# Kernel tuning notes

Hardware: AMD Instinct MI355X
Metric: run time of the kernel (lower is better)

The kernel has to match this reference:

```python
import jax, jax.numpy as jnp
import numpy as np

T, I, H = 30, 100, 256  # seq_len, input_size, hidden_size (hard-coded in the module)


def setup_inputs() -> dict:
    key = jax.random.key(0)
    ks = jax.random.split(key, 16)
    B = 512
    N = B * 10  # LSTM batch after view(-1, 30, 100)
    w = lambda k, shape: (jax.random.normal(k, shape, dtype=jnp.float32) * 0.05)
    return {
        "x": jax.random.normal(ks[0], (B, 10, T, I), dtype=jnp.float32),
        "h0": jax.random.normal(ks[1], (2, N, H), dtype=jnp.float32),
        "c0": jax.random.normal(ks[2], (2, N, H), dtype=jnp.float32),
        # PyTorch LSTM params, gate order i,f,g,o; forward and backward directions
        "W_ih_f": w(ks[3], (4 * H, I)),
        "W_hh_f": w(ks[4], (4 * H, H)),
        "b_ih_f": w(ks[5], (4 * H,)),
        "b_hh_f": w(ks[6], (4 * H,)),
        "W_ih_b": w(ks[7], (4 * H, I)),
        "W_hh_b": w(ks[8], (4 * H, H)),
        "b_ih_b": w(ks[9], (4 * H,)),
        "b_hh_b": w(ks[10], (4 * H,)),
        # head: Linear(2560,64) -> Dropout(eval: identity) -> Linear(64,5) -> Softmax
        "W1": w(ks[11], (64, 10 * 256)),
        "b1": w(ks[12], (64,)),
        "W2": w(ks[13], (5, 64)),
        "b2": w(ks[14], (5,)),
    }


def _run_dir(xg, h, c, W_hh):
    """Scan an LSTM direction. xg: [T, N, 4H] precomputed input gates. Returns final h."""
    def step(carry, g_x):
        h, c = carry
        g = g_x + h @ W_hh.T
        i, f, gg, o = jnp.split(g, 4, axis=-1)
        c = jax.nn.sigmoid(f) * c + jax.nn.sigmoid(i) * jnp.tanh(gg)
        h = jax.nn.sigmoid(o) * jnp.tanh(c)
        return (h, c), None
    (h, c), _ = jax.lax.scan(step, (h, c), xg)
    return h


def reference(x, h0, c0, W_ih_f, W_hh_f, b_ih_f, b_hh_f,
              W_ih_b, W_hh_b, b_ih_b, b_hh_b, W1, b1, W2, b2):
    B = x.shape[0]
    xr = x.reshape(-1, T, I)              # [N, 30, 100]
    xs = jnp.transpose(xr, (1, 0, 2))     # [T, N, I] time-major
    # precompute input contributions to gates for all timesteps (one big GEMM)
    xg_f = jnp.einsum('tni,gi->tng', xs, W_ih_f) + b_ih_f + b_hh_f
    xg_b = jnp.einsum('tni,gi->tng', xs[::-1], W_ih_b) + b_ih_b + b_hh_b
    hF = _run_dir(xg_f, h0[0], c0[0], W_hh_f)  # fwd hidden at t=T-1 -> output[:, -1, :256]
    hB = _run_dir(xg_b, h0[1], c0[1], W_hh_b)  # bwd hidden at t=0  -> output[:, 0, 256:]
    # output[:, -1, :128] = hF[:, :128]; output[:, 0, -128:] = hB[:, 128:256]
    x_fea = jnp.concatenate(
        [hF[:, :128].reshape(B, 10, 128), hB[:, 128:256].reshape(B, 10, 128)], axis=-1)
    flat = x_fea.reshape(B, -1)           # [B, 2560]
    z = flat @ W1.T + b1                  # Dropout(0.5) is identity in eval
    logits = z @ W2.T + b2
    y_pred = jax.nn.softmax(logits, axis=-1)
    return (y_pred, x_fea)
```

## Files before the change

### kernel.cpp

```cpp
#include <hip/hip_runtime.h>

typedef __bf16 bf16_t;
typedef __bf16 bf16x8 __attribute__((ext_vector_type(8)));
typedef float f32x4 __attribute__((ext_vector_type(4)));
typedef unsigned long long u64;

#define TSEQ 30
#define ISZ  100
#define HSZ  256
#define NB   5120
#define BATCH 512
#define G4   1024
#define TILE 320
#define NBGRP 16
#define CH   10240
#define SLABX (4 * CH)
#define SLABH (8 * CH)

__device__ __forceinline__ float fsig(float x)  { return 1.0f / (1.0f + __expf(-x)); }
__device__ __forceinline__ float ftanh(float x) { return 2.0f / (1.0f + __expf(-2.0f * x)) - 1.0f; }

__global__ void prep_weights(const float* __restrict__ Wih_f, const float* __restrict__ Whh_f,
                             const float* __restrict__ bih_f, const float* __restrict__ bhh_f,
                             const float* __restrict__ Wih_b, const float* __restrict__ Whh_b,
                             const float* __restrict__ bih_b, const float* __restrict__ bhh_b,
                             bf16_t* __restrict__ Wf, float* __restrict__ bias)
{
    int idx = blockIdx.x * 256 + threadIdx.x;
    if (idx >= 2 * G4 * 384) return;
    int d = idx / (G4 * 384);
    int r = (idx / 384) % G4;
    int k = idx % 384;
    int h = r >> 2, gate = r & 3;
    int grow = gate * HSZ + h;
    const float* Wih = d ? Wih_b : Wih_f;
    const float* Whh = d ? Whh_b : Whh_f;
    float v;
    if (k < ISZ)       v = Wih[grow * ISZ + k];
    else if (k < 128)  v = 0.0f;
    else               v = Whh[grow * HSZ + (k - 128)];
    int mf = r >> 4, lr = r & 15;
    int ks = k >> 5, lq = (k >> 3) & 3, e = k & 7;
    size_t o = ((((size_t)d * 64 + mf) * 12 + ks) * 64 + lq * 16 + lr) * 8 + e;
    Wf[o] = (bf16_t)v;
    if (k == 0) {
        const float* bih = d ? bih_b : bih_f;
        const float* bhh = d ? bhh_b : bhh_f;
        bias[d * G4 + r] = bih[grow] + bhh[grow];
    }
}

__global__ void prep_x(const float* __restrict__ x, bf16_t* __restrict__ xBf)
{
    int idx = blockIdx.x * 256 + threadIdx.x;
    if (idx >= NBGRP * TSEQ * SLABX) return;
    int e    = idx & 7;
    int lane = (idx >> 3) & 63;
    int i2   = idx >> 9;
    int nblk = i2 % 20; i2 /= 20;
    int ks   = i2 & 3;  i2 >>= 2;
    int t    = i2 % TSEQ;
    int bgrp = i2 / TSEQ;
    int n = bgrp * TILE + nblk * 16 + (lane & 15);
    int k = ks * 32 + (lane >> 4) * 8 + e;
    float v = (k < ISZ) ? x[(size_t)n * (TSEQ * ISZ) + t * ISZ + k] : 0.0f;
    xBf[idx] = (bf16_t)v;
}

__global__ void prep_state(const float* __restrict__ h0, bf16_t* __restrict__ hA)
{
    int idx = blockIdx.x * 256 + threadIdx.x;
    if (idx >= 2 * NBGRP * SLABH) return;
    int e    = idx & 7;
    int lane = (idx >> 3) & 63;
    int i2   = idx >> 9;
    int nblk = i2 % 20; i2 /= 20;
    int ksh  = i2 & 7;  i2 >>= 3;
    int bgrp = i2 & 15;
    int dir  = i2 >> 4;
    int col = bgrp * TILE + nblk * 16 + (lane & 15);
    int hid = ksh * 32 + (lane >> 4) * 8 + e;
    hA[idx] = (bf16_t)h0[((size_t)dir * NB + col) * HSZ + hid];
}

__global__ void prep_c(const float* __restrict__ c0, float* __restrict__ cws)
{
    int idx = blockIdx.x * 256 + threadIdx.x;
    if (idx >= 256 * 512 * 20) return;
    int m   = idx & 3;
    int nf  = (idx >> 2) % 5;
    int tid = (idx / 20) & 511;
    int bid = idx / (20 * 512);
    int msub = bid >> 5, dir = (bid >> 4) & 1, bgrp = bid & 15;
    int lane = tid & 63, mw = (tid >> 6) >> 2, nw = (tid >> 6) & 3;
    int lr = lane & 15, lq = lane >> 4;
    int col = bgrp * TILE + nw * 80 + nf * 16 + lr;
    int hid = msub * 32 + mw * 16 + m * 4 + lq;
    cws[idx] = c0[((size_t)dir * NB + col) * HSZ + hid];
}

__global__ void prep_w1t(const float* __restrict__ W1, float* __restrict__ W1T)
{
    int idx = blockIdx.x * 256 + threadIdx.x;
    if (idx >= 2560 * 64) return;
    int k = idx / 64, j = idx % 64;
    W1T[k * 64 + j] = W1[j * 2560 + k];
}

__device__ __forceinline__ void wave_wait(unsigned* flag, unsigned tgt)
{
    if ((threadIdx.x & 63) == 0) {
        while (__hip_atomic_fetch_add(flag, 0u, __ATOMIC_RELAXED, __HIP_MEMORY_SCOPE_AGENT) < tgt)
            __builtin_amdgcn_s_sleep(1);
    }
    __builtin_amdgcn_wave_barrier();
    __builtin_amdgcn_sched_barrier(0);
}

template<bool FAST>
__device__ void run_steps(const bf16_t* __restrict__ xBf,
                          bf16_t* __restrict__ hA, bf16_t* __restrict__ hB,
                          bf16_t* __restrict__ hfin,
                          const bf16_t* wL, bf16_t* pkL, unsigned* flags,
                          f32x4* c4, const float4* bq,
                          int dir, int bgrp, int msub,
                          int tid, int lane, int mw, int nw, int lr, int lq)
{
    const unsigned fo = (unsigned)(nw * 5 * 512 + lane * 8);
    const bf16_t* wp = wL + (mw * 4 * 12) * 512 + lane * 8;

#pragma unroll 1
    for (int t = 0; t < TSEQ; ++t) {
        const bf16_t* hs = (t & 1) ? hB : hA;
        bf16_t*       hw = (t & 1) ? hA : hB;
        const int tx = dir ? (TSEQ - 1 - t) : t;
        const bf16_t* xp = xBf + (size_t)(bgrp * TSEQ + tx) * SLABX + fo;
        const bf16_t* hp = hs + (size_t)(dir * NBGRP + bgrp) * SLABH + fo;

        f32x4 acc[4][5] = {};
#pragma unroll
        for (int c = 0; c < 4; ++c) {
            bf16x8 b[5];
#pragma unroll
            for (int nf = 0; nf < 5; ++nf)
                b[nf] = *(const bf16x8*)(xp + nf * 512);
            bf16x8 a[4];
#pragma unroll
            for (int m = 0; m < 4; ++m)
                a[m] = *(const bf16x8*)(wp + (m * 12 + c) * 512);
#pragma unroll
            for (int m = 0; m < 4; ++m)
#pragma unroll
                for (int nf = 0; nf < 5; ++nf)
                    acc[m][nf] = __builtin_amdgcn_mfma_f32_16x16x32_bf16(a[m], b[nf], acc[m][nf], 0, 0, 0);
            xp += CH;
        }
        if (FAST)
            asm volatile("buffer_inv sc0" ::: "memory");
#pragma unroll
        for (int c = 0; c < 8; ++c) {
            if (c != msub) wave_wait(flags + c * 16, (unsigned)t);
            bf16x8 b[5];
#pragma unroll
            for (int nf = 0; nf < 5; ++nf) {
                const bf16_t* src = hp + nf * 512;
                if (FAST) {
                    b[nf] = *(const bf16x8*)src;
                } else {
                    union { u64 q[2]; bf16x8 v; } u;
                    u.q[0] = __hip_atomic_load((const u64*)src,       __ATOMIC_RELAXED, __HIP_MEMORY_SCOPE_AGENT);
                    u.q[1] = __hip_atomic_load((const u64*)(src + 4), __ATOMIC_RELAXED, __HIP_MEMORY_SCOPE_AGENT);
                    b[nf] = u.v;
                }
            }
            bf16x8 a[4];
#pragma unroll
            for (int m = 0; m < 4; ++m)
                a[m] = *(const bf16x8*)(wp + (m * 12 + c + 4) * 512);
#pragma unroll
            for (int m = 0; m < 4; ++m)
#pragma unroll
                for (int nf = 0; nf < 5; ++nf)
                    acc[m][nf] = __builtin_amdgcn_mfma_f32_16x16x32_bf16(a[m], b[nf], acc[m][nf], 0, 0, 0);
            hp += CH;
        }

        if (t < TSEQ - 1) {
#pragma unroll
            for (int m = 0; m < 4; ++m) {
                float4 bb = bq[m];
                int hl = mw * 16 + m * 4 + lq;
#pragma unroll
                for (int nf = 0; nf < 5; ++nf) {
                    f32x4 g = acc[m][nf];
                    float gi = fsig(g[0] + bb.x);
                    float gf = fsig(g[1] + bb.y);
                    float gz = ftanh(g[2] + bb.z);
                    float go = fsig(g[3] + bb.w);
                    float cn = gf * c4[nf][m] + gi * gz;
                    c4[nf][m] = cn;
                    pkL[(nw * 5 + nf) * 512 + ((hl >> 3) * 16 + lr) * 8 + (hl & 7)]
                        = (bf16_t)(go * ftanh(cn));
                }
            }
            __syncthreads();
            bf16_t* dstb = hw + (size_t)(dir * NBGRP + bgrp) * SLABH + (size_t)msub * CH;
            if (FAST) {
                uint4* dst = (uint4*)dstb;
                const uint4* src = (const uint4*)pkL;
                for (int i = tid; i < 1280; i += 512) dst[i] = src[i];
            } else {
                u64* dst = (u64*)dstb;
                const u64* src = (const u64*)pkL;
                for (int i = tid; i < 2560; i += 512)
                    __hip_atomic_store(&dst[i], src[i], __ATOMIC_RELAXED, __HIP_MEMORY_SCOPE_AGENT);
            }
            __syncthreads();
            if (tid == 0)
                __hip_atomic_fetch_add(flags + msub * 16, 1u,
                    FAST ? __ATOMIC_RELAXED : __ATOMIC_RELEASE, __HIP_MEMORY_SCOPE_AGENT);
        } else {
#pragma unroll
            for (int m = 0; m < 4; ++m) {
                float4 bb = bq[m];
#pragma unroll
                for (int nf = 0; nf < 5; ++nf) {
                    f32x4 g = acc[m][nf];
                    float gi = fsig(g[0] + bb.x);
                    float gf = fsig(g[1] + bb.y);
                    float gz = ftanh(g[2] + bb.z);
                    float go = fsig(g[3] + bb.w);
                    float cn = gf * c4[nf][m] + gi * gz;
                    float hn = go * ftanh(cn);
                    int col = bgrp * TILE + nw * 80 + nf * 16 + lr;
                    int hid = msub * 32 + mw * 16 + m * 4 + lq;
                    hfin[((size_t)dir * NB + col) * HSZ + hid] = (bf16_t)hn;
                }
            }
        }
    }
}

__global__ __launch_bounds__(512, 1)
void lstm_persist(const bf16_t* __restrict__ Wf, const float* __restrict__ bias,
                  const bf16_t* __restrict__ xBf, const float* __restrict__ cws,
                  bf16_t* __restrict__ hA, bf16_t* __restrict__ hB,
                  bf16_t* __restrict__ hfin, unsigned* __restrict__ bar,
                  unsigned* __restrict__ xccA)
{
    __shared__ __align__(16) bf16_t wL[8 * 12 * 512];
    __shared__ __align__(16) bf16_t pkL[CH];
    __shared__ int sFast;

    const int bid  = blockIdx.x;
    const int msub = bid >> 5;
    const int dir  = (bid >> 4) & 1;
    const int bgrp = bid & 15;
    const int tid  = threadIdx.x;
    const int lane = tid & 63;
    const int mw   = (tid >> 6) >> 2;
    const int nw   = (tid >> 6) & 3;
    const int lr   = lane & 15;
    const int lq   = lane >> 4;

    {
        const uint4* wsrc = (const uint4*)(Wf + ((size_t)dir * 64 + msub * 8) * 12 * 512);
        uint4* wdst = (uint4*)wL;
        for (int i = tid; i < 6144; i += 512) wdst[i] = wsrc[i];
    }
    const float* cp = cws + ((size_t)bid * 512 + tid) * 20;
    f32x4 c4[5];
#pragma unroll
    for (int nf = 0; nf < 5; ++nf) c4[nf] = *(const f32x4*)(cp + nf * 4);
    float4 bq[4];
#pragma unroll
    for (int m = 0; m < 4; ++m)
        bq[m] = *(const float4*)(bias + dir * G4 + (msub * 32 + mw * 16 + m * 4 + lq) * 4);

    unsigned* flags  = bar + (dir * NBGRP + bgrp) * 128;
    unsigned* mybarX = bar + 32 * 128 + (dir * NBGRP + bgrp) * 16;

    unsigned xcc;
    asm volatile("s_getreg_b32 %0, hwreg(HW_REG_XCC_ID)" : "=s"(xcc));
    if (tid == 0) {
        __hip_atomic_store(&xccA[bid], xcc, __ATOMIC_RELAXED, __HIP_MEMORY_SCOPE_AGENT);
        __hip_atomic_fetch_add(mybarX, 1u, __ATOMIC_RELEASE, __HIP_MEMORY_SCOPE_AGENT);
        while (__hip_atomic_fetch_add(mybarX, 0u, __ATOMIC_RELAXED, __HIP_MEMORY_SCOPE_AGENT) < 8u)
            __builtin_amdgcn_s_sleep(1);
        int ok = (xcc < 8u) ? 1 : 0;
        for (int m2 = 0; m2 < 8; ++m2) {
            unsigned v = __hip_atomic_load(&xccA[m2 * 32 + dir * 16 + bgrp],
                                           __ATOMIC_RELAXED, __HIP_MEMORY_SCOPE_AGENT);
            ok &= (v == xcc) ? 1 : 0;
        }
        sFast = ok;
    }
    __syncthreads();

    if (sFast)
        run_steps<true>(xBf, hA, hB, hfin, wL, pkL, flags, c4, bq,
                        dir, bgrp, msub, tid, lane, mw, nw, lr, lq);
    else
        run_steps<false>(xBf, hA, hB, hfin, wL, pkL, flags, c4, bq,
                         dir, bgrp, msub, tid, lane, mw, nw, lr, lq);
}

__global__ __launch_bounds__(256)
void head_kernel(const bf16_t* __restrict__ hfin, const float* __restrict__ W1T,
                 const float* __restrict__ b1, const float* __restrict__ W2,
                 const float* __restrict__ b2, float* __restrict__ out)
{
    __shared__ float flat_s[2560];
    __shared__ float partial[4][64];
    __shared__ float zs[64];
    __shared__ float ls[5];
    __shared__ float es[5];
    int b = blockIdx.x, tid = threadIdx.x;
    const bf16_t* hF = hfin;
    const bf16_t* hB = hfin + (size_t)NB * HSZ;
    float* xfea = out + BATCH * 5 + (size_t)b * 2560;

    for (int j = tid; j < 2560; j += 256) {
        int s = j >> 8, c = j & 255;
        int n = b * 10 + s;
        float v = (c < 128) ? (float)hF[(size_t)n * HSZ + c] : (float)hB[(size_t)n * HSZ + c];
        flat_s[j] = v;
        xfea[j] = v;
    }
    __syncthreads();
    int j = tid & 63, q = tid >> 6;
    float sum = 0.0f;
    for (int k = q * 640; k < (q + 1) * 640; ++k) sum += flat_s[k] * W1T[k * 64 + j];
    partial[q][j] = sum;
    __syncthreads();
    if (tid < 64) zs[tid] = partial[0][tid] + partial[1][tid] + partial[2][tid] + partial[3][tid] + b1[tid];
    __syncthreads();
    if (tid < 5) {
        float l = b2[tid];
        for (int k = 0; k < 64; ++k) l += zs[k] * W2[tid * 64 + k];
        ls[tid] = l;
    }
    __syncthreads();
    if (tid < 5) {
        float m = ls[0];
        for (int k = 1; k < 5; ++k) m = fmaxf(m, ls[k]);
        es[tid] = __expf(ls[tid] - m);
    }
    __syncthreads();
    if (tid < 5) {
        float s5 = es[0] + es[1] + es[2] + es[3] + es[4];
        out[b * 5 + tid] = es[tid] / s5;
    }
}

extern "C" void kernel_launch(void* const* d_in, const int* in_sizes, int n_in,
                              void* d_out, int out_size, void* d_ws, size_t ws_size,
                              hipStream_t stream) {
    const float* x     = (const float*)d_in[0];
    const float* h0    = (const float*)d_in[1];
    const float* c0    = (const float*)d_in[2];
    const float* Wih_f = (const float*)d_in[3];
    const float* Whh_f = (const float*)d_in[4];
    const float* bih_f = (const float*)d_in[5];
    const float* bhh_f = (const float*)d_in[6];
    const float* Wih_b = (const float*)d_in[7];
    const float* Whh_b = (const float*)d_in[8];
    const float* bih_b = (const float*)d_in[9];
    const float* bhh_b = (const float*)d_in[10];
    const float* W1    = (const float*)d_in[11];
    const float* b1    = (const float*)d_in[12];
    const float* W2    = (const float*)d_in[13];
    const float* b2    = (const float*)d_in[14];
    float* out = (float*)d_out;

    uintptr_t ws = (uintptr_t)d_ws;
    bf16_t*   Wf   = (bf16_t*)(ws);
    float*    bias = (float*)(ws + 1572864);
    bf16_t*   xBf  = (bf16_t*)(ws + 1581056);
    bf16_t*   hAb  = (bf16_t*)(ws + 40902656);
    bf16_t*   hBb  = (bf16_t*)(ws + 46145536);
    bf16_t*   hfin = (bf16_t*)(ws + 51388416);
    float*    W1T  = (float*)(ws + 56631296);
    float*    cws  = (float*)(ws + 57286656);
    unsigned* bar  = (unsigned*)(ws + 67772416);
    unsigned* xccA = (unsigned*)(ws + 67790848);

    hipMemsetAsync((void*)bar, 0, 18432, stream);

    prep_weights<<<(2 * G4 * 384 + 255) / 256, 256, 0, stream>>>(
        Wih_f, Whh_f, bih_f, bhh_f, Wih_b, Whh_b, bih_b, bhh_b, Wf, bias);
    prep_x<<<(NBGRP * TSEQ * SLABX + 255) / 256, 256, 0, stream>>>(x, xBf);
    prep_state<<<(2 * NBGRP * SLABH + 255) / 256, 256, 0, stream>>>(h0, hAb);
    prep_c<<<(256 * 512 * 20 + 255) / 256, 256, 0, stream>>>(c0, cws);
    prep_w1t<<<(2560 * 64 + 255) / 256, 256, 0, stream>>>(W1, W1T);

    lstm_persist<<<256, 512, 0, stream>>>(Wf, bias, xBf, cws, hAb, hBb, hfin, bar, xccA);
    head_kernel<<<BATCH, 256, 0, stream>>>(hfin, W1T, b1, W2, b2, out);
}
```

Before: 467.0 us.

## Split blocks across both directions and replace per-chunk waits with per-wave flags

Each persistent block now handles both LSTM directions: half its threads work on forward and half on backward, each owning 16 hidden units instead of 32. Per-chunk flag waits become a single ballot-based batch wait over 16 per-wave flags. The LDS staging buffer and its two __syncthreads are dropped, and h values are written straight to global with a per-wave flag increment. This is meant to shorten the per-step cross-block synchronization path, at the cost of scattered 2-byte global stores and more flags to poll per step.

```diff
diff --git a/kernel.cpp b/kernel.cpp
--- a/kernel.cpp
+++ b/kernel.cpp
@@ -87,16 +87,19 @@
 {
     int idx = blockIdx.x * 256 + threadIdx.x;
     if (idx >= 256 * 512 * 20) return;
-    int m   = idx & 3;
-    int nf  = (idx >> 2) % 5;
-    int tid = (idx / 20) & 511;
-    int bid = idx / (20 * 512);
-    int msub = bid >> 5, dir = (bid >> 4) & 1, bgrp = bid & 15;
-    int lane = tid & 63, mw = (tid >> 6) >> 2, nw = (tid >> 6) & 3;
+    int cell = idx % 20;
+    int m    = cell / 10, nf = cell % 10;
+    int tid  = (idx / 20) & 511;
+    int bid  = idx / (20 * 512);
+    int msub = bid >> 4, bgrp = bid & 15;
+    int dirc = tid >> 8;
+    int ctid = tid & 255;
+    int wavec = ctid >> 6, lane = ctid & 63;
+    int mw = wavec >> 1, nw = wavec & 1;
     int lr = lane & 15, lq = lane >> 4;
-    int col = bgrp * TILE + nw * 80 + nf * 16 + lr;
-    int hid = msub * 32 + mw * 16 + m * 4 + lq;
-    cws[idx] = c0[((size_t)dir * NB + col) * HSZ + hid];
+    int col = bgrp * TILE + (nw * 10 + nf) * 16 + lr;
+    int hid = msub * 16 + mw * 8 + m * 4 + lq;
+    cws[idx] = c0[((size_t)dirc * NB + col) * HSZ + hid];
 }
 
 __global__ void prep_w1t(const float* __restrict__ W1, float* __restrict__ W1T)
@@ -107,13 +110,16 @@
     W1T[k * 64 + j] = W1[j * 2560 + k];
 }
 
-__device__ __forceinline__ void wave_wait(unsigned* flag, unsigned tgt)
-{
-    if ((threadIdx.x & 63) == 0) {
-        while (__hip_atomic_fetch_add(flag, 0u, __ATOMIC_RELAXED, __HIP_MEMORY_SCOPE_AGENT) < tgt)
-            __builtin_amdgcn_s_sleep(1);
-    }
-    __builtin_amdgcn_wave_barrier();
+__device__ __forceinline__ void batch_wait(unsigned* flags, unsigned tgt, int lane)
+{
+    while (true) {
+        unsigned v = tgt;
+        if (lane < 16)
+            v = __hip_atomic_fetch_add(flags + lane * 16, 0u,
+                                       __ATOMIC_RELAXED, __HIP_MEMORY_SCOPE_AGENT);
+        if (__ballot(v >= tgt) == ~0ull) break;
+        __builtin_amdgcn_s_sleep(8);
+    }
     __builtin_amdgcn_sched_barrier(0);
 }
 
@@ -121,48 +127,56 @@
 __device__ void run_steps(const bf16_t* __restrict__ xBf,
                           bf16_t* __restrict__ hA, bf16_t* __restrict__ hB,
                           bf16_t* __restrict__ hfin,
-                          const bf16_t* wL, bf16_t* pkL, unsigned* flags,
-                          f32x4* c4, const float4* bq,
-                          int dir, int bgrp, int msub,
+                          const bf16_t* wL, unsigned* myflags, unsigned* ownflag,
+                          float* cst, const float4* bq,
+                          int dirc, int bgrp, int msub,
                           int tid, int lane, int mw, int nw, int lr, int lq)
 {
-    const unsigned fo = (unsigned)(nw * 5 * 512 + lane * 8);
-    const bf16_t* wp = wL + (mw * 4 * 12) * 512 + lane * 8;
+    const unsigned fo = (unsigned)(nw * 10 * 512 + lane * 8);
+    const bf16_t* wp = wL + ((size_t)(dirc * 4 + mw * 2) * 12) * 512 + lane * 8;
+    const size_t slab = (size_t)(dirc * NBGRP + bgrp) * SLABH;
+
+    unsigned sb[2];
+#pragma unroll
+    for (int m = 0; m < 2; ++m) {
+        int hid = msub * 16 + mw * 8 + m * 4 + lq;
+        sb[m] = (unsigned)((hid >> 5) * CH + (((hid & 31) >> 3) * 16 + lr) * 8 + (hid & 7));
+    }
 
 #pragma unroll 1
     for (int t = 0; t < TSEQ; ++t) {
         const bf16_t* hs = (t & 1) ? hB : hA;
         bf16_t*       hw = (t & 1) ? hA : hB;
-        const int tx = dir ? (TSEQ - 1 - t) : t;
+        const int tx = dirc ? (TSEQ - 1 - t) : t;
         const bf16_t* xp = xBf + (size_t)(bgrp * TSEQ + tx) * SLABX + fo;
-        const bf16_t* hp = hs + (size_t)(dir * NBGRP + bgrp) * SLABH + fo;
-
-        f32x4 acc[4][5] = {};
+        const bf16_t* hp = hs + slab + fo;
+
+        f32x4 acc0[10] = {}, acc1[10] = {};
 #pragma unroll
         for (int c = 0; c < 4; ++c) {
-            bf16x8 b[5];
-#pragma unroll
-            for (int nf = 0; nf < 5; ++nf)
+            bf16x8 b[10];
+#pragma unroll
+            for (int nf = 0; nf < 10; ++nf)
                 b[nf] = *(const bf16x8*)(xp + nf * 512);
-            bf16x8 a[4];
-#pragma unroll
-            for (int m = 0; m < 4; ++m)
-                a[m] = *(const bf16x8*)(wp + (m * 12 + c) * 512);
-#pragma unroll
-            for (int m = 0; m < 4; ++m)
-#pragma unroll
-                for (int nf = 0; nf < 5; ++nf)
-                    acc[m][nf] = __builtin_amdgcn_mfma_f32_16x16x32_bf16(a[m], b[nf], acc[m][nf], 0, 0, 0);
+            bf16x8 a0 = *(const bf16x8*)(wp + (0 * 12 + c) * 512);
+            bf16x8 a1 = *(const bf16x8*)(wp + (1 * 12 + c) * 512);
+#pragma unroll
+            for (int nf = 0; nf < 10; ++nf) {
+                acc0[nf] = __builtin_amdgcn_mfma_f32_16x16x32_bf16(a0, b[nf], acc0[nf], 0, 0, 0);
+                acc1[nf] = __builtin_amdgcn_mfma_f32_16x16x32_bf16(a1, b[nf], acc1[nf], 0, 0, 0);
+            }
             xp += CH;
         }
+
+        batch_wait(myflags, 4u * (unsigned)t, lane);
         if (FAST)
             asm volatile("buffer_inv sc0" ::: "memory");
+
 #pragma unroll
         for (int c = 0; c < 8; ++c) {
-            if (c != msub) wave_wait(flags + c * 16, (unsigned)t);
-            bf16x8 b[5];
-#pragma unroll
-            for (int nf = 0; nf < 5; ++nf) {
+            bf16x8 b[10];
+#pragma unroll
+            for (int nf = 0; nf < 10; ++nf) {
                 const bf16_t* src = hp + nf * 512;
                 if (FAST) {
                     b[nf] = *(const bf16x8*)src;
@@ -173,68 +187,61 @@
                     b[nf] = u.v;
                 }
             }
-            bf16x8 a[4];
-#pragma unroll
-            for (int m = 0; m < 4; ++m)
-                a[m] = *(const bf16x8*)(wp + (m * 12 + c + 4) * 512);
-#pragma unroll
-            for (int m = 0; m < 4; ++m)
-#pragma unroll
-                for (int nf = 0; nf < 5; ++nf)
-                    acc[m][nf] = __builtin_amdgcn_mfma_f32_16x16x32_bf16(a[m], b[nf], acc[m][nf], 0, 0, 0);
+            bf16x8 a0 = *(const bf16x8*)(wp + (0 * 12 + 4 + c) * 512);
+            bf16x8 a1 = *(const bf16x8*)(wp + (1 * 12 + 4 + c) * 512);
+#pragma unroll
+            for (int nf = 0; nf < 10; ++nf) {
+                acc0[nf] = __builtin_amdgcn_mfma_f32_16x16x32_bf16(a0, b[nf], acc0[nf], 0, 0, 0);
+                acc1[nf] = __builtin_amdgcn_mfma_f32_16x16x32_bf16(a1, b[nf], acc1[nf], 0, 0, 0);
+            }
             hp += CH;
         }
 
         if (t < TSEQ - 1) {
-#pragma unroll
-            for (int m = 0; m < 4; ++m) {
+            bf16_t* hwp = hw + slab;
+#pragma unroll
+            for (int m = 0; m < 2; ++m) {
                 float4 bb = bq[m];
-                int hl = mw * 16 + m * 4 + lq;
-#pragma unroll
-                for (int nf = 0; nf < 5; ++nf) {
-                    f32x4 g = acc[m][nf];
+#pragma unroll
+                for (int nf = 0; nf < 10; ++nf) {
+                    f32x4 g = m ? acc1[nf] : acc0[nf];
                     float gi = fsig(g[0] + bb.x);
                     float gf = fsig(g[1] + bb.y);
                     float gz = ftanh(g[2] + bb.z);
                     float go = fsig(g[3] + bb.w);
-                    float cn = gf * c4[nf][m] + gi * gz;
-                    c4[nf][m] = cn;
-                    pkL[(nw * 5 + nf) * 512 + ((hl >> 3) * 16 + lr) * 8 + (hl & 7)]
-                        = (bf16_t)(go * ftanh(cn));
+                    float cn = gf * cst[m * 10 + nf] + gi * gz;
+                    cst[m * 10 + nf] = cn;
+                    bf16_t hv = (bf16_t)(go * ftanh(cn));
+                    unsigned off = sb[m] + (unsigned)((nw * 10 + nf) * 512);
+                    if (FAST) {
+                        hwp[off] = hv;
+                    } else {
+                        union { bf16_t h; unsigned short u; } cv; cv.h = hv;
+                        __hip_atomic_store((unsigned short*)(hwp + off), cv.u,
+                                           __ATOMIC_RELAXED, __HIP_MEMORY_SCOPE_AGENT);
+                    }
                 }
             }
-            __syncthreads();
-            bf16_t* dstb = hw + (size_t)(dir * NBGRP + bgrp) * SLABH + (size_t)msub * CH;
-            if (FAST) {
-                uint4* dst = (uint4*)dstb;
-                const uint4* src = (const uint4*)pkL;
-                for (int i = tid; i < 1280; i += 512) dst[i] = src[i];
-            } else {
-                u64* dst = (u64*)dstb;
-                const u64* src = (const u64*)pkL;
-                for (int i = tid; i < 2560; i += 512)
-                    __hip_atomic_store(&dst[i], src[i], __ATOMIC_RELAXED, __HIP_MEMORY_SCOPE_AGENT);
-            }
-            __syncthreads();
-            if (tid == 0)
-                __hip_atomic_fetch_add(flags + msub * 16, 1u,
+            if (FAST) asm volatile("s_waitcnt vmcnt(0)" ::: "memory");
+            if ((tid & 63) == 0)
+                __hip_atomic_fetch_add(ownflag, 1u,
                     FAST ? __ATOMIC_RELAXED : __ATOMIC_RELEASE, __HIP_MEMORY_SCOPE_AGENT);
         } else {
 #pragma unroll
-            for (int m = 0; m < 4; ++m) {
+            for (int m = 0; m < 2; ++m) {
                 float4 bb = bq[m];
-#pragma unroll
-                for (int nf = 0; nf < 5; ++nf) {
-                    f32x4 g = acc[m][nf];
+                int hid = msub * 16 + mw * 8 + m * 4 + lq;
+#pragma unroll
+                for (int nf = 0; nf < 10; ++nf) {
+                    f32x4 g = m ? acc1[nf] : acc0[nf];
                     float gi = fsig(g[0] + bb.x);
                     float gf = fsig(g[1] + bb.y);
                     float gz = ftanh(g[2] + bb.z);
                     float go = fsig(g[3] + bb.w);
-                    float cn = gf * c4[nf][m] + gi * gz;
+                    float cn = gf * cst[m * 10 + nf] + gi * gz;
                     float hn = go * ftanh(cn);
-                    int col = bgrp * TILE + nw * 80 + nf * 16 + lr;
-                    int hid = msub * 32 + mw * 16 + m * 4 + lq;
-                    hfin[((size_t)dir * NB + col) * HSZ + hid] = (bf16_t)hn;
+                    int col = bgrp * TILE + (nw * 10 + nf) * 16 + lr;
+                    hfin[((size_t)dirc * NB + col) * HSZ + hid] = (bf16_t)hn;
                 }
             }
         }
@@ -248,48 +255,59 @@
                   bf16_t* __restrict__ hfin, unsigned* __restrict__ bar,
                   unsigned* __restrict__ xccA)
 {
-    __shared__ __align__(16) bf16_t wL[8 * 12 * 512];
-    __shared__ __align__(16) bf16_t pkL[CH];
+    __shared__ __align__(16) bf16_t wL[2 * 4 * 12 * 512];
     __shared__ int sFast;
 
     const int bid  = blockIdx.x;
-    const int msub = bid >> 5;
-    const int dir  = (bid >> 4) & 1;
+    const int msub = bid >> 4;
     const int bgrp = bid & 15;
     const int tid  = threadIdx.x;
-    const int lane = tid & 63;
-    const int mw   = (tid >> 6) >> 2;
-    const int nw   = (tid >> 6) & 3;
+    const int dirc = tid >> 8;
+    const int ctid = tid & 255;
+    const int wavec = ctid >> 6;
+    const int lane = ctid & 63;
+    const int mw   = wavec >> 1;
+    const int nw   = wavec & 1;
     const int lr   = lane & 15;
     const int lq   = lane >> 4;
 
     {
-        const uint4* wsrc = (const uint4*)(Wf + ((size_t)dir * 64 + msub * 8) * 12 * 512);
         uint4* wdst = (uint4*)wL;
-        for (int i = tid; i < 6144; i += 512) wdst[i] = wsrc[i];
+        for (int i = tid; i < 6144; i += 512) {
+            int d = i / 3072, off = i % 3072;
+            const uint4* src = (const uint4*)(Wf + ((size_t)(d * 64 + msub * 4) * 12) * 512);
+            wdst[d * 3072 + off] = src[off];
+        }
     }
     const float* cp = cws + ((size_t)bid * 512 + tid) * 20;
-    f32x4 c4[5];
-#pragma unroll
-    for (int nf = 0; nf < 5; ++nf) c4[nf] = *(const f32x4*)(cp + nf * 4);
-    float4 bq[4];
-#pragma unroll
-    for (int m = 0; m < 4; ++m)
-        bq[m] = *(const float4*)(bias + dir * G4 + (msub * 32 + mw * 16 + m * 4 + lq) * 4);
-
-    unsigned* flags  = bar + (dir * NBGRP + bgrp) * 128;
-    unsigned* mybarX = bar + 32 * 128 + (dir * NBGRP + bgrp) * 16;
+    float cst[20];
+#pragma unroll
+    for (int i = 0; i < 5; ++i) {
+        float4 v = *(const float4*)(cp + i * 4);
+        cst[i * 4 + 0] = v.x; cst[i * 4 + 1] = v.y;
+        cst[i * 4 + 2] = v.z; cst[i * 4 + 3] = v.w;
+    }
+    float4 bq[2];
+#pragma unroll
+    for (int m = 0; m < 2; ++m) {
+        int hid = msub * 16 + mw * 8 + m * 4 + lq;
+        bq[m] = *(const float4*)(bias + dirc * G4 + hid * 4);
+    }
+
+    unsigned* myflags = bar + (dirc * NBGRP + bgrp) * 256;
+    unsigned* ownflag = myflags + msub * 16;
+    unsigned* gbar    = bar + 8192 + bgrp * 16;
 
     unsigned xcc;
     asm volatile("s_getreg_b32 %0, hwreg(HW_REG_XCC_ID)" : "=s"(xcc));
     if (tid == 0) {
         __hip_atomic_store(&xccA[bid], xcc, __ATOMIC_RELAXED, __HIP_MEMORY_SCOPE_AGENT);
-        __hip_atomic_fetch_add(mybarX, 1u, __ATOMIC_RELEASE, __HIP_MEMORY_SCOPE_AGENT);
-        while (__hip_atomic_fetch_add(mybarX, 0u, __ATOMIC_RELAXED, __HIP_MEMORY_SCOPE_AGENT) < 8u)
+        __hip_atomic_fetch_add(gbar, 1u, __ATOMIC_RELEASE, __HIP_MEMORY_SCOPE_AGENT);
+        while (__hip_atomic_fetch_add(gbar, 0u, __ATOMIC_RELAXED, __HIP_MEMORY_SCOPE_AGENT) < 16u)
             __builtin_amdgcn_s_sleep(1);
         int ok = (xcc < 8u) ? 1 : 0;
-        for (int m2 = 0; m2 < 8; ++m2) {
-            unsigned v = __hip_atomic_load(&xccA[m2 * 32 + dir * 16 + bgrp],
+        for (int m2 = 0; m2 < 16; ++m2) {
+            unsigned v = __hip_atomic_load(&xccA[m2 * 16 + bgrp],
                                            __ATOMIC_RELAXED, __HIP_MEMORY_SCOPE_AGENT);
             ok &= (v == xcc) ? 1 : 0;
         }
@@ -298,11 +316,11 @@
     __syncthreads();
 
     if (sFast)
-        run_steps<true>(xBf, hA, hB, hfin, wL, pkL, flags, c4, bq,
-                        dir, bgrp, msub, tid, lane, mw, nw, lr, lq);
+        run_steps<true>(xBf, hA, hB, hfin, wL, myflags, ownflag, cst, bq,
+                        dirc, bgrp, msub, tid, lane, mw, nw, lr, lq);
     else
-        run_steps<false>(xBf, hA, hB, hfin, wL, pkL, flags, c4, bq,
-                         dir, bgrp, msub, tid, lane, mw, nw, lr, lq);
+        run_steps<false>(xBf, hA, hB, hfin, wL, myflags, ownflag, cst, bq,
+                         dirc, bgrp, msub, tid, lane, mw, nw, lr, lq);
 }
 
 __global__ __launch_bounds__(256)
@@ -383,9 +401,9 @@
     float*    W1T  = (float*)(ws + 56631296);
     float*    cws  = (float*)(ws + 57286656);
     unsigned* bar  = (unsigned*)(ws + 67772416);
-    unsigned* xccA = (unsigned*)(ws + 67790848);
-
-    hipMemsetAsync((void*)bar, 0, 18432, stream);
+    unsigned* xccA = (unsigned*)(ws + 67809280);
+
+    hipMemsetAsync((void*)bar, 0, 40960, stream);
 
     prep_weights<<<(2 * G4 * 384 + 255) / 256, 256, 0, stream>>>(
         Wih_f, Whh_f, bih_f, bhh_f, Wih_b, Whh_b, bih_b, bhh_b, Wf, bias);
```

Result: slower. 694.1 us (+48.6%).

## Replace block barriers with per-wave flag publishing and batched flag polling

Applied to the files above, without the earlier changes.

Each wave now copies its own slice of the packed hidden state to global memory and increments the block's flag itself, so the two __syncthreads around the copy disappear. The flag target becomes 8 per step per block. Consumers poll all eight producer flags at once, using lanes 0-7 and a ballot, before reading any of the recurrent state, instead of spinning on each flag one at a time inside the chunk loop. This is meant to cut intra-block barrier stalls and serial polling latency on the recurrent critical path, but it gives up overlapping flag waits with the early MFMA chunks. It also relies on each wave's LDS slice matching what that same wave wrote.

```diff
diff --git a/kernel.cpp b/kernel.cpp
--- a/kernel.cpp
+++ b/kernel.cpp
@@ -107,13 +107,16 @@
     W1T[k * 64 + j] = W1[j * 2560 + k];
 }
 
-__device__ __forceinline__ void wave_wait(unsigned* flag, unsigned tgt)
-{
-    if ((threadIdx.x & 63) == 0) {
-        while (__hip_atomic_fetch_add(flag, 0u, __ATOMIC_RELAXED, __HIP_MEMORY_SCOPE_AGENT) < tgt)
-            __builtin_amdgcn_s_sleep(1);
-    }
-    __builtin_amdgcn_wave_barrier();
+__device__ __forceinline__ void batch_wait8(unsigned* flags, unsigned tgt, int lane)
+{
+    while (true) {
+        unsigned v = tgt;
+        if (lane < 8)
+            v = __hip_atomic_fetch_add(flags + lane * 16, 0u,
+                                       __ATOMIC_RELAXED, __HIP_MEMORY_SCOPE_AGENT);
+        if (__ballot(v >= tgt) == ~0ull) break;
+        __builtin_amdgcn_s_sleep(4);
+    }
     __builtin_amdgcn_sched_barrier(0);
 }
 
@@ -121,13 +124,15 @@
 __device__ void run_steps(const bf16_t* __restrict__ xBf,
                           bf16_t* __restrict__ hA, bf16_t* __restrict__ hB,
                           bf16_t* __restrict__ hfin,
-                          const bf16_t* wL, bf16_t* pkL, unsigned* flags,
+                          const bf16_t* wL, bf16_t* pkL,
+                          unsigned* flags, unsigned* ownflag,
                           f32x4* c4, const float4* bq,
                           int dir, int bgrp, int msub,
                           int tid, int lane, int mw, int nw, int lr, int lq)
 {
     const unsigned fo = (unsigned)(nw * 5 * 512 + lane * 8);
     const bf16_t* wp = wL + (mw * 4 * 12) * 512 + lane * 8;
+    const size_t slab = (size_t)(dir * NBGRP + bgrp) * SLABH;
 
 #pragma unroll 1
     for (int t = 0; t < TSEQ; ++t) {
@@ -135,7 +140,7 @@
         bf16_t*       hw = (t & 1) ? hA : hB;
         const int tx = dir ? (TSEQ - 1 - t) : t;
         const bf16_t* xp = xBf + (size_t)(bgrp * TSEQ + tx) * SLABX + fo;
-        const bf16_t* hp = hs + (size_t)(dir * NBGRP + bgrp) * SLABH + fo;
+        const bf16_t* hp = hs + slab + fo;
 
         f32x4 acc[4][5] = {};
 #pragma unroll
@@ -155,11 +160,13 @@
                     acc[m][nf] = __builtin_amdgcn_mfma_f32_16x16x32_bf16(a[m], b[nf], acc[m][nf], 0, 0, 0);
             xp += CH;
         }
+
+        batch_wait8(flags, 8u * (unsigned)t, lane);
         if (FAST)
             asm volatile("buffer_inv sc0" ::: "memory");
+
 #pragma unroll
         for (int c = 0; c < 8; ++c) {
-            if (c != msub) wave_wait(flags + c * 16, (unsigned)t);
             bf16x8 b[5];
 #pragma unroll
             for (int nf = 0; nf < 5; ++nf) {
@@ -203,21 +210,24 @@
                         = (bf16_t)(go * ftanh(cn));
                 }
             }
-            __syncthreads();
-            bf16_t* dstb = hw + (size_t)(dir * NBGRP + bgrp) * SLABH + (size_t)msub * CH;
-            if (FAST) {
-                uint4* dst = (uint4*)dstb;
-                const uint4* src = (const uint4*)pkL;
-                for (int i = tid; i < 1280; i += 512) dst[i] = src[i];
-            } else {
-                u64* dst = (u64*)dstb;
-                const u64* src = (const u64*)pkL;
-                for (int i = tid; i < 2560; i += 512)
-                    __hip_atomic_store(&dst[i], src[i], __ATOMIC_RELAXED, __HIP_MEMORY_SCOPE_AGENT);
+            asm volatile("s_waitcnt lgkmcnt(0)" ::: "memory");
+            __builtin_amdgcn_sched_barrier(0);
+            bf16_t* dstb = hw + slab + (size_t)msub * CH;
+#pragma unroll
+            for (int nf = 0; nf < 5; ++nf) {
+                unsigned so = (unsigned)((nw * 5 + nf) * 512 + mw * 256 + lane * 4);
+                uint2 v = *(const uint2*)(pkL + so);
+                if (FAST) {
+                    *(uint2*)(dstb + so) = v;
+                } else {
+                    union { uint2 d; u64 q; } cv; cv.d = v;
+                    __hip_atomic_store((u64*)(dstb + so), cv.q,
+                                       __ATOMIC_RELAXED, __HIP_MEMORY_SCOPE_AGENT);
+                }
             }
-            __syncthreads();
-            if (tid == 0)
-                __hip_atomic_fetch_add(flags + msub * 16, 1u,
+            asm volatile("s_waitcnt vmcnt(0)" ::: "memory");
+            if ((tid & 63) == 0)
+                __hip_atomic_fetch_add(ownflag, 1u,
                     FAST ? __ATOMIC_RELAXED : __ATOMIC_RELEASE, __HIP_MEMORY_SCOPE_AGENT);
         } else {
 #pragma unroll
@@ -277,8 +287,9 @@
     for (int m = 0; m < 4; ++m)
         bq[m] = *(const float4*)(bias + dir * G4 + (msub * 32 + mw * 16 + m * 4 + lq) * 4);
 
-    unsigned* flags  = bar + (dir * NBGRP + bgrp) * 128;
-    unsigned* mybarX = bar + 32 * 128 + (dir * NBGRP + bgrp) * 16;
+    unsigned* flags   = bar + (dir * NBGRP + bgrp) * 128;
+    unsigned* ownflag = flags + msub * 16;
+    unsigned* mybarX  = bar + 32 * 128 + (dir * NBGRP + bgrp) * 16;
 
     unsigned xcc;
     asm volatile("s_getreg_b32 %0, hwreg(HW_REG_XCC_ID)" : "=s"(xcc));
@@ -298,10 +309,10 @@
     __syncthreads();
 
     if (sFast)
-        run_steps<true>(xBf, hA, hB, hfin, wL, pkL, flags, c4, bq,
+        run_steps<true>(xBf, hA, hB, hfin, wL, pkL, flags, ownflag, c4, bq,
                         dir, bgrp, msub, tid, lane, mw, nw, lr, lq);
     else
-        run_steps<false>(xBf, hA, hB, hfin, wL, pkL, flags, c4, bq,
+        run_steps<false>(xBf, hA, hB, hfin, wL, pkL, flags, ownflag, c4, bq,
                          dir, bgrp, msub, tid, lane, mw, nw, lr, lq);
 }
 
```

Measured after the change: 641.6 us. 1.37x slower.
